# Performance work log

Hardware: AMD Instinct MI355X
Metric: run time of the kernel (lower is better)

Reference implementation:

```python
import jax, jax.numpy as jnp
import numpy as np

N_NODES = 50000
N_EDGES = 600000
D = 128


def gcn_conv(x, src, dst, W, b, n_nodes):
    """PyG GCNConv: h = D^-1/2 (A+I) D^-1/2 (x @ W) + b, messages src->dst."""
    h = x @ W  # [N, out]
    # add self loops (weight 1)
    loop = jnp.arange(n_nodes, dtype=src.dtype)
    s = jnp.concatenate([src, loop])
    d = jnp.concatenate([dst, loop])
    w = jnp.ones(s.shape[0], dtype=x.dtype)
    deg = jax.ops.segment_sum(w, d, num_segments=n_nodes)  # in-degree at target
    dinv = jnp.where(deg > 0, jax.lax.rsqrt(deg), 0.0).astype(x.dtype)
    norm = dinv[s] * w * dinv[d]  # [E+N]
    msg = h[s] * norm[:, None]  # gather + scale
    out = jax.ops.segment_sum(msg, d, num_segments=n_nodes)  # scatter-add
    return out + b


def setup_inputs() -> dict:
    key = jax.random.key(0)
    k1, k2, k3, k4, k5, k6 = jax.random.split(key, 6)
    x = jax.random.normal(k1, (N_NODES, D), dtype=jnp.float32)
    edge_index = jax.random.randint(k2, (2, N_EDGES), 0, N_NODES, dtype=jnp.int64)
    s = (1.0 / np.sqrt(D))
    W1 = jax.random.normal(k3, (D, D), dtype=jnp.float32) * s
    b1 = jnp.zeros((D,), dtype=jnp.float32)
    W2 = jax.random.normal(k4, (D, D), dtype=jnp.float32) * s
    b2 = jnp.zeros((D,), dtype=jnp.float32)
    return {"x": x, "edge_index": edge_index, "W1": W1, "b1": b1, "W2": W2, "b2": b2}


def reference(x, edge_index, W1, b1, W2, b2):
    src, dst = edge_index[0], edge_index[1]
    # two GCN layers (order=2), ReLU activation; dropout is identity at eval
    o1 = jax.nn.relu(gcn_conv(x, src, dst, W1, b1, N_NODES))
    o2 = jax.nn.relu(gcn_conv(x, src, dst, W2, b2, N_NODES))
    # combine_mode='mean'
    return 0.5 * (o1 + o2)
```

## Files before the change

kernel.cpp:

```cpp
#include <hip/hip_runtime.h>
#include <hip/hip_bf16.h>

#define N_NODES 50000
#define N_EDGES 600000
#define D 128
#define CAP 64
#define ZSTRIDE 136

typedef __attribute__((ext_vector_type(8))) short bfrag;
typedef __attribute__((ext_vector_type(4))) float ffrag;

__device__ __forceinline__ short bf16bits(float f) {
    __hip_bfloat16 h = __float2bfloat16(f);
    return *reinterpret_cast<short*>(&h);
}
__device__ __forceinline__ float bfbits2float(short b) {
    unsigned u = ((unsigned)(unsigned short)b) << 16;
    return __uint_as_float(u);
}

__device__ __forceinline__ unsigned norm_cnt(unsigned raw) {
    return raw - (raw >= 0x80000000u ? 0xAAAAAAAAu : 0u);
}

__global__ void fill_kernel(const int* __restrict__ src, const int* __restrict__ dst,
                            unsigned* __restrict__ cnt, int* __restrict__ srcs) {
    int e = blockIdx.x * 256 + threadIdx.x;
    if (e < N_EDGES) {
        int d = dst[e];
        unsigned slot = norm_cnt(atomicAdd(&cnt[d], 1u));
        if (slot < CAP) srcs[d * CAP + slot] = src[e];
    }
}

__global__ __launch_bounds__(256) void dxw_kernel(
    const float* __restrict__ x,
    const float* __restrict__ W1, const float* __restrict__ W2,
    const unsigned* __restrict__ cnt,
    __hip_bfloat162* __restrict__ xs, int* __restrict__ srcs,
    short* __restrict__ wpack)
{
    int idx = blockIdx.x * 256 + threadIdx.x;

    int node = idx >> 6;
    unsigned deg = norm_cnt(cnt[node]);
    float dv = rsqrtf((float)(deg + 1));
    float2 v = ((const float2*)x)[idx];
    __hip_bfloat162 h;
    h.x = __float2bfloat16(dv * v.x);
    h.y = __float2bfloat16(dv * v.y);
    xs[idx] = h;

    if ((idx & 63) == 0) {
        unsigned n8 = (deg + 7u) & ~7u;
        n8 = n8 < CAP ? n8 : CAP;
        for (unsigned s2 = deg; s2 < n8; ++s2) srcs[node * CAP + s2] = N_NODES;
    }

    if (idx < 64) {
        __hip_bfloat162 z0;
        z0.x = __float2bfloat16(0.f);
        z0.y = __float2bfloat16(0.f);
        xs[N_NODES * 64 + idx] = z0;
    }

    if (idx < 2 * 8 * 4 * 64 * 8) {
        int j  = idx & 7;
        int l  = (idx >> 3) & 63;
        int ks = (idx >> 9) & 3;
        int c  = (idx >> 11) & 7;
        int m  = (idx >> 14) & 1;
        int k = ks * 32 + (l >> 4) * 8 + j;
        int n = c * 16 + (l & 15);
        const float* W = m ? W2 : W1;
        wpack[idx] = bf16bits(W[k * D + n]);
    }
}

__global__ __launch_bounds__(256, 5) void fused_kernel(
    const unsigned* __restrict__ cnt,
    const int* __restrict__ srcs,
    const __hip_bfloat162* __restrict__ xs,
    const short* __restrict__ wpack,
    const float* __restrict__ b1,
    const float* __restrict__ b2,
    float* __restrict__ out)
{
    __shared__ __align__(16) short zs16[16 * ZSTRIDE];
    const int base = blockIdx.x * 16;
    const int t = threadIdx.x;
    const int lane = t & 63;
    const int g = t >> 6;
    const int p = lane & 15;
    const int q = lane >> 4;

    for (int rr = 0; rr < 4; ++rr) {
        const int r = g * 4 + rr;
        const int node = base + r;
        unsigned deg = norm_cnt(cnt[node]);
        const float dv = rsqrtf((float)(deg + 1));
        unsigned n8 = (deg + 7u) & ~7u;
        n8 = n8 < CAP ? n8 : CAP;
        const int rb = node * CAP;

        float acc[8];
#pragma unroll
        for (int j = 0; j < 8; ++j) acc[j] = 0.f;

        for (unsigned e = 0; e < n8; e += 8) {
            int s0 = srcs[rb + e + q];
            int s1 = srcs[rb + e + 4 + q];
            bfrag v0 = ((const bfrag*)(xs + s0 * 64))[p];
            bfrag v1 = ((const bfrag*)(xs + s1 * 64))[p];
#pragma unroll
            for (int j = 0; j < 8; ++j)
                acc[j] += bfbits2float(v0[j]) + bfbits2float(v1[j]);
        }

#pragma unroll
        for (int j = 0; j < 8; ++j) {
            acc[j] += __shfl_xor(acc[j], 16, 64);
            acc[j] += __shfl_xor(acc[j], 32, 64);
        }

        if (q == 0) {
            bfrag vs = ((const bfrag*)(xs + node * 64))[p];
            bfrag zo;
#pragma unroll
            for (int j = 0; j < 8; ++j)
                zo[j] = bf16bits(dv * (acc[j] + bfbits2float(vs[j])));
            *(bfrag*)&zs16[r * ZSTRIDE + p * 8] = zo;
        }
    }
    __syncthreads();

    const int m16 = lane & 15;
    const int quad = lane >> 4;
    const int c0 = 2 * g;
    const int c1 = 2 * g + 1;

    ffrag acc00 = {0.f, 0.f, 0.f, 0.f};
    ffrag acc01 = {0.f, 0.f, 0.f, 0.f};
    ffrag acc10 = {0.f, 0.f, 0.f, 0.f};
    ffrag acc11 = {0.f, 0.f, 0.f, 0.f};

#pragma unroll
    for (int ks = 0; ks < 4; ++ks) {
        bfrag a = *(const bfrag*)&zs16[m16 * ZSTRIDE + ks * 32 + quad * 8];

        bfrag b00 = *(const bfrag*)&wpack[((((0 * 8 + c0) * 4 + ks) * 64 + lane) * 8)];
        bfrag b01 = *(const bfrag*)&wpack[((((0 * 8 + c1) * 4 + ks) * 64 + lane) * 8)];
        bfrag b10 = *(const bfrag*)&wpack[((((1 * 8 + c0) * 4 + ks) * 64 + lane) * 8)];
        bfrag b11 = *(const bfrag*)&wpack[((((1 * 8 + c1) * 4 + ks) * 64 + lane) * 8)];

        acc00 = __builtin_amdgcn_mfma_f32_16x16x32_bf16(a, b00, acc00, 0, 0, 0);
        acc01 = __builtin_amdgcn_mfma_f32_16x16x32_bf16(a, b01, acc01, 0, 0, 0);
        acc10 = __builtin_amdgcn_mfma_f32_16x16x32_bf16(a, b10, acc10, 0, 0, 0);
        acc11 = __builtin_amdgcn_mfma_f32_16x16x32_bf16(a, b11, acc11, 0, 0, 0);
    }

    const int n0 = c0 * 16 + m16;
    const int n1 = c1 * 16 + m16;
    const float b1n0 = b1[n0], b1n1 = b1[n1];
    const float b2n0 = b2[n0], b2n1 = b2[n1];
#pragma unroll
    for (int reg = 0; reg < 4; ++reg) {
        int row = quad * 4 + reg;
        int node = base + row;
        float o0 = 0.5f * (fmaxf(acc00[reg] + b1n0, 0.f) + fmaxf(acc10[reg] + b2n0, 0.f));
        float o1 = 0.5f * (fmaxf(acc01[reg] + b1n1, 0.f) + fmaxf(acc11[reg] + b2n1, 0.f));
        out[node * D + n0] = o0;
        out[node * D + n1] = o1;
    }
}

extern "C" void kernel_launch(void* const* d_in, const int* in_sizes, int n_in,
                              void* d_out, int out_size, void* d_ws, size_t ws_size,
                              hipStream_t stream) {
    const float* x  = (const float*)d_in[0];
    const int*   ei = (const int*)d_in[1];
    const float* W1 = (const float*)d_in[2];
    const float* b1 = (const float*)d_in[3];
    const float* W2 = (const float*)d_in[4];
    const float* b2 = (const float*)d_in[5];
    float* out = (float*)d_out;

    const int* src = ei;
    const int* dst = ei + N_EDGES;

    char* ws = (char*)d_ws;
    unsigned* cnt  = (unsigned*)(ws + 0);
    int*      srcs = (int*)(ws + 200704);
    __hip_bfloat162* xs = (__hip_bfloat162*)(ws + 13000704);
    short*    wpack = (short*)(ws + 25800960);

    fill_kernel<<<(N_EDGES + 255) / 256, 256, 0, stream>>>(src, dst, cnt, srcs);
    dxw_kernel<<<12500, 256, 0, stream>>>(x, W1, W2, cnt, xs, srcs, wpack);
    fused_kernel<<<N_NODES / 16, 256, 0, stream>>>(cnt, srcs, xs, wpack, b1, b2, out);
}
```

Measured before the change: 152.9 us.

## Interleave gathers for four nodes per wave to raise memory-level parallelism

The aggregation loop now processes all four destination nodes of a wave together. Each node's source list is loaded once into a register and broadcast with shuffles, and eight row gathers per iteration are issued before any accumulation. Inactive nodes are padded to the zero row, and source indices are clamped to the valid range. The goal is to hide gather latency by keeping more loads in flight, at the cost of more registers, which drops the occupancy hint from 5 to 4, and of wasted gathers when the four nodes have uneven degrees.

```diff
diff --git a/kernel.cpp b/kernel.cpp
--- a/kernel.cpp
+++ b/kernel.cpp
@@ -77,7 +77,7 @@
     }
 }
 
-__global__ __launch_bounds__(256, 5) void fused_kernel(
+__global__ __launch_bounds__(256, 4) void fused_kernel(
     const unsigned* __restrict__ cnt,
     const int* __restrict__ srcs,
     const __hip_bfloat162* __restrict__ xs,
@@ -94,41 +94,68 @@
     const int p = lane & 15;
     const int q = lane >> 4;
 
+    int sreg[4];
+    unsigned n8[4];
+    float dvr[4];
+    bfrag vself[4];
+#pragma unroll
+    for (int rr = 0; rr < 4; ++rr) {
+        const int node = base + g * 4 + rr;
+        unsigned deg = norm_cnt(cnt[node]);
+        dvr[rr] = rsqrtf((float)(deg + 1));
+        unsigned m = (deg + 7u) & ~7u;
+        n8[rr] = m < CAP ? m : CAP;
+        sreg[rr] = srcs[node * CAP + lane];
+        vself[rr] = ((const bfrag*)(xs + node * 64))[p];
+    }
+    unsigned mx = n8[0] > n8[1] ? n8[0] : n8[1];
+    unsigned mx2 = n8[2] > n8[3] ? n8[2] : n8[3];
+    mx = mx > mx2 ? mx : mx2;
+
+    float acc[4][8];
+#pragma unroll
+    for (int rr = 0; rr < 4; ++rr)
+#pragma unroll
+        for (int j = 0; j < 8; ++j) acc[rr][j] = 0.f;
+
+    for (unsigned e = 0; e < mx; e += 8) {
+        int s0v[4], s1v[4];
+#pragma unroll
+        for (int rr = 0; rr < 4; ++rr) {
+            int i0 = __shfl(sreg[rr], (int)e + q, 64);
+            int i1 = __shfl(sreg[rr], (int)e + 4 + q, 64);
+            bool act = e < n8[rr];
+            i0 = i0 < 0 ? 0 : (i0 > N_NODES ? N_NODES : i0);
+            i1 = i1 < 0 ? 0 : (i1 > N_NODES ? N_NODES : i1);
+            s0v[rr] = act ? i0 : N_NODES;
+            s1v[rr] = act ? i1 : N_NODES;
+        }
+        bfrag v0[4], v1[4];
+#pragma unroll
+        for (int rr = 0; rr < 4; ++rr) {
+            v0[rr] = ((const bfrag*)(xs + s0v[rr] * 64))[p];
+            v1[rr] = ((const bfrag*)(xs + s1v[rr] * 64))[p];
+        }
+#pragma unroll
+        for (int rr = 0; rr < 4; ++rr)
+#pragma unroll
+            for (int j = 0; j < 8; ++j)
+                acc[rr][j] += bfbits2float(v0[rr][j]) + bfbits2float(v1[rr][j]);
+    }
+
+#pragma unroll
     for (int rr = 0; rr < 4; ++rr) {
         const int r = g * 4 + rr;
-        const int node = base + r;
-        unsigned deg = norm_cnt(cnt[node]);
-        const float dv = rsqrtf((float)(deg + 1));
-        unsigned n8 = (deg + 7u) & ~7u;
-        n8 = n8 < CAP ? n8 : CAP;
-        const int rb = node * CAP;
-
-        float acc[8];
-#pragma unroll
-        for (int j = 0; j < 8; ++j) acc[j] = 0.f;
-
-        for (unsigned e = 0; e < n8; e += 8) {
-            int s0 = srcs[rb + e + q];
-            int s1 = srcs[rb + e + 4 + q];
-            bfrag v0 = ((const bfrag*)(xs + s0 * 64))[p];
-            bfrag v1 = ((const bfrag*)(xs + s1 * 64))[p];
+#pragma unroll
+        for (int j = 0; j < 8; ++j) {
+            acc[rr][j] += __shfl_xor(acc[rr][j], 16, 64);
+            acc[rr][j] += __shfl_xor(acc[rr][j], 32, 64);
+        }
+        if (q == 0) {
+            bfrag zo;
 #pragma unroll
             for (int j = 0; j < 8; ++j)
-                acc[j] += bfbits2float(v0[j]) + bfbits2float(v1[j]);
-        }
-
-#pragma unroll
-        for (int j = 0; j < 8; ++j) {
-            acc[j] += __shfl_xor(acc[j], 16, 64);
-            acc[j] += __shfl_xor(acc[j], 32, 64);
-        }
-
-        if (q == 0) {
-            bfrag vs = ((const bfrag*)(xs + node * 64))[p];
-            bfrag zo;
-#pragma unroll
-            for (int j = 0; j < 8; ++j)
-                zo[j] = bf16bits(dv * (acc[j] + bfbits2float(vs[j])));
+                zo[j] = bf16bits(dvr[rr] * (acc[rr][j] + bfbits2float(vself[rr][j])));
             *(bfrag*)&zs16[r * ZSTRIDE + p * 8] = zo;
         }
     }
```

After: 151.6 us. About the same (-0.9%).
